# Kernel tuning notes

Hardware: AMD Instinct MI355X
Metric: run time of the kernel (lower is better)

The kernel has to match this reference:

```python
import jax, jax.numpy as jnp
import numpy as np

GAMMA = 1.0


def setup_inputs() -> dict:
    key = jax.random.key(0)
    kx, ky = jax.random.split(key)
    x = jax.random.normal(kx, (8192, 128), dtype=jnp.float32)
    y = jax.random.normal(ky, (8192, 128), dtype=jnp.float32)
    return {"x": x, "y": y}


def reference(x, y):
    # RBF kernel K[i,j] = exp(-gamma * ||x_i - y_j||^2)
    x2 = jnp.sum(x * x, axis=1)              # [N]
    y2 = jnp.sum(y * y, axis=1)              # [M]
    xy = jnp.einsum('nd,md->nm', x, y)       # [N, M] GEMM
    sq = x2[:, None] + y2[None, :] - 2.0 * xy
    sq = jnp.maximum(sq, 0.0)                # guard tiny negatives from cancellation
    return jnp.exp(-GAMMA * sq)
```

## Files before the change

### kernel.cpp

```cpp
#include <hip/hip_runtime.h>
#include <hip/hip_bf16.h>

typedef __bf16 bf16x8 __attribute__((ext_vector_type(8)));
typedef float f32x4 __attribute__((ext_vector_type(4)));
typedef unsigned short us4 __attribute__((ext_vector_type(4)));

#define NLOG2E -1.44269504088896340736f

__device__ __forceinline__ unsigned short f2bf(float f) {
    unsigned u = __float_as_uint(f);
    u += 0x7fffu + ((u >> 16) & 1u);
    return (unsigned short)(u >> 16);
}

__global__ __launch_bounds__(256)
void rbf_prep(const float* __restrict__ X, const float* __restrict__ Y,
              unsigned short* __restrict__ Xb, unsigned short* __restrict__ Yb,
              float* __restrict__ x2n, float* __restrict__ y2n) {
    const int b = blockIdx.x;
    const float* src = (b < 128) ? X : Y;
    unsigned short* db = (b < 128) ? Xb : Yb;
    float* dn = (b < 128) ? x2n : y2n;
    const int r0 = (b & 127) * 64;
    const int t = threadIdx.x;
    const f32x4* s4 = (const f32x4*)(src + (size_t)r0 * 128);
#pragma unroll
    for (int i = 0; i < 8; ++i) {
        int idx = i * 256 + t;
        int r = idx >> 5, c4 = idx & 31;
        f32x4 v = s4[idx];
        us4 o;
        o.x = f2bf(v[0]); o.y = f2bf(v[1]); o.z = f2bf(v[2]); o.w = f2bf(v[3]);
        int pc = (c4 >> 1) ^ (r & 7);
        *(us4*)&db[(size_t)(r0 + r) * 128 + pc * 8 + (c4 & 1) * 4] = o;
    }
    if (t < 64) {
        const f32x4* row = (const f32x4*)(src + (size_t)(r0 + t) * 128);
        float s = 0.f;
#pragma unroll
        for (int c = 0; c < 32; ++c) {
            f32x4 v = row[c];
            s += v[0] * v[0] + v[1] * v[1] + v[2] * v[2] + v[3] * v[3];
        }
        dn[r0 + t] = NLOG2E * s;
    }
}

__global__ __launch_bounds__(256, 5)
void rbf_main(const unsigned short* __restrict__ Xb, const unsigned short* __restrict__ Yb,
              const float* __restrict__ x2n, const float* __restrict__ y2n,
              float* __restrict__ O) {
    __shared__ __align__(16) char smem[32768];
    unsigned short* Ab = (unsigned short*)smem;
    unsigned short* Bb = (unsigned short*)(smem + 16384);

    const int t = threadIdx.x, l = t & 63, w = t >> 6;
    const int col0 = blockIdx.x * 64, row0 = blockIdx.y * 64;

    const char* gA = (const char*)(Xb + (size_t)row0 * 128);
    const char* gB = (const char*)(Yb + (size_t)col0 * 128);
#pragma unroll
    for (int j = 0; j < 4; ++j) {
        int base = (w * 4 + j) * 1024;
        __builtin_amdgcn_global_load_lds(
            (const __attribute__((address_space(1))) void*)(gA + base + l * 16),
            (__attribute__((address_space(3))) void*)(smem + base), 16, 0, 0);
        __builtin_amdgcn_global_load_lds(
            (const __attribute__((address_space(1))) void*)(gB + base + l * 16),
            (__attribute__((address_space(3))) void*)(smem + 16384 + base), 16, 0, 0);
    }

    const int lr = l & 15, q = l >> 4;
    const int wr = (w >> 1) * 32, wc = (w & 1) * 32;

    f32x4 xn[2]; float yn[2];
#pragma unroll
    for (int m = 0; m < 2; ++m) xn[m] = *(const f32x4*)&x2n[row0 + wr + m * 16 + q * 4];
#pragma unroll
    for (int n = 0; n < 2; ++n) yn[n] = y2n[col0 + wc + n * 16 + lr];

    __syncthreads();

    f32x4 acc[2][2] = {};
#pragma unroll
    for (int k = 0; k < 4; ++k) {
        bf16x8 af[2], bv[2];
#pragma unroll
        for (int m = 0; m < 2; ++m) {
            int R = wr + m * 16 + lr;
            af[m] = *(const bf16x8*)((const char*)Ab + R * 256 + (((k << 2) + q) ^ (R & 7)) * 16);
        }
#pragma unroll
        for (int n = 0; n < 2; ++n) {
            int R = wc + n * 16 + lr;
            bv[n] = *(const bf16x8*)((const char*)Bb + R * 256 + (((k << 2) + q) ^ (R & 7)) * 16);
        }
#pragma unroll
        for (int m = 0; m < 2; ++m)
#pragma unroll
            for (int n = 0; n < 2; ++n)
                acc[m][n] = __builtin_amdgcn_mfma_f32_16x16x32_bf16(af[m], bv[n], acc[m][n], 0, 0, 0);
    }

    __syncthreads();

    float* Ol = (float*)(smem + w * 4096);
#pragma unroll
    for (int m = 0; m < 2; ++m) {
#pragma unroll
        for (int n = 0; n < 2; ++n) {
            int col = n * 16 + lr;
            int lc = col >> 2;
            float ynv = yn[n];
#pragma unroll
            for (int i = 0; i < 4; ++i) {
                int row = m * 16 + q * 4 + i;
                float arg = fmaf(-2.0f * NLOG2E, acc[m][n][i], xn[m][i] + ynv);
                arg = fminf(arg, 0.f);
                int pc = (lc ^ row) & 7;
                Ol[row * 32 + pc * 4 + (col & 3)] = exp2f(arg);
            }
        }
    }

#pragma unroll
    for (int it = 0; it < 4; ++it) {
        int r = it * 8 + (l >> 3);
        int lc2 = l & 7;
        int pc = lc2 ^ (r & 7);
        f32x4 v = *(const f32x4*)((const char*)Ol + r * 128 + pc * 16);
        *(float4*)&O[(size_t)(row0 + wr + r) * 8192 + col0 + wc + lc2 * 4] = *(float4*)&v;
    }
}

extern "C" void kernel_launch(void* const* d_in, const int* in_sizes, int n_in,
                              void* d_out, int out_size, void* d_ws, size_t ws_size,
                              hipStream_t stream) {
    const float* X = (const float*)d_in[0];
    const float* Y = (const float*)d_in[1];
    float* O = (float*)d_out;
    const int N = in_sizes[0] / 128;
    const int M = in_sizes[1] / 128;
    unsigned short* Xb = (unsigned short*)d_ws;
    unsigned short* Yb = Xb + (size_t)N * 128;
    float* x2n = (float*)(Yb + (size_t)M * 128);
    float* y2n = x2n + N;
    rbf_prep<<<dim3((N + M) / 64), 256, 0, stream>>>(X, Y, Xb, Yb, x2n, y2n);
    rbf_main<<<dim3(M / 64, N / 64), 256, 0, stream>>>(Xb, Yb, x2n, y2n, O);
}
```

Before: 285.2 us.

## Widen output tile to 64x128 with 32x32 MFMA and direct stores

Each block now covers 128 columns instead of 64, and the GEMM switches from 16x16x32 MFMAs to 32x32x16 MFMAs so one A fragment is reused across two B fragments. The LDS-staged transposed output write is removed. Results are stored straight from the MFMA accumulator layout as 32 consecutive floats per row segment. This cuts LDS traffic, one barrier and the per-block setup, at the cost of more shared memory, lower occupancy (launch bound 3) and possibly less coalesced stores.

```diff
diff --git a/kernel.cpp b/kernel.cpp
--- a/kernel.cpp
+++ b/kernel.cpp
@@ -3,9 +3,11 @@
 
 typedef __bf16 bf16x8 __attribute__((ext_vector_type(8)));
 typedef float f32x4 __attribute__((ext_vector_type(4)));
+typedef float f32x16 __attribute__((ext_vector_type(16)));
 typedef unsigned short us4 __attribute__((ext_vector_type(4)));
 
-#define NLOG2E -1.44269504088896340736f
+#define NLOG2E  -1.44269504088896340736f
+#define TWOLOG2E 2.88539008177792681472f
 
 __device__ __forceinline__ unsigned short f2bf(float f) {
     unsigned u = __float_as_uint(f);
@@ -46,16 +48,14 @@
     }
 }
 
-__global__ __launch_bounds__(256, 5)
+__global__ __launch_bounds__(256, 3)
 void rbf_main(const unsigned short* __restrict__ Xb, const unsigned short* __restrict__ Yb,
               const float* __restrict__ x2n, const float* __restrict__ y2n,
-              float* __restrict__ O) {
-    __shared__ __align__(16) char smem[32768];
-    unsigned short* Ab = (unsigned short*)smem;
-    unsigned short* Bb = (unsigned short*)(smem + 16384);
+              float* __restrict__ O, int ldo) {
+    __shared__ __align__(16) char smem[49152];
 
     const int t = threadIdx.x, l = t & 63, w = t >> 6;
-    const int col0 = blockIdx.x * 64, row0 = blockIdx.y * 64;
+    const int col0 = blockIdx.x * 128, row0 = blockIdx.y * 64;
 
     const char* gA = (const char*)(Xb + (size_t)row0 * 128);
     const char* gB = (const char*)(Yb + (size_t)col0 * 128);
@@ -65,71 +65,57 @@
         __builtin_amdgcn_global_load_lds(
             (const __attribute__((address_space(1))) void*)(gA + base + l * 16),
             (__attribute__((address_space(3))) void*)(smem + base), 16, 0, 0);
+    }
+#pragma unroll
+    for (int j = 0; j < 8; ++j) {
+        int base = (w * 8 + j) * 1024;
         __builtin_amdgcn_global_load_lds(
             (const __attribute__((address_space(1))) void*)(gB + base + l * 16),
             (__attribute__((address_space(3))) void*)(smem + 16384 + base), 16, 0, 0);
     }
 
-    const int lr = l & 15, q = l >> 4;
-    const int wr = (w >> 1) * 32, wc = (w & 1) * 32;
+    const int ln = l & 31, hi = l >> 5;
+    const int wr = (w >> 1) * 32, wcw = (w & 1) * 64;
 
-    f32x4 xn[2]; float yn[2];
+    f32x4 xv[4];
 #pragma unroll
-    for (int m = 0; m < 2; ++m) xn[m] = *(const f32x4*)&x2n[row0 + wr + m * 16 + q * 4];
+    for (int g = 0; g < 4; ++g)
+        xv[g] = *(const f32x4*)&x2n[row0 + wr + 8 * g + 4 * hi];
+    float ynp[2];
 #pragma unroll
-    for (int n = 0; n < 2; ++n) yn[n] = y2n[col0 + wc + n * 16 + lr];
+    for (int nf = 0; nf < 2; ++nf)
+        ynp[nf] = y2n[col0 + wcw + nf * 32 + ln];
 
     __syncthreads();
 
-    f32x4 acc[2][2] = {};
+    f32x16 acc0 = {}, acc1 = {};
+    const int RA = wr + ln;
+    const int C0 = wcw + ln;
+    const int C1 = wcw + 32 + ln;
 #pragma unroll
-    for (int k = 0; k < 4; ++k) {
-        bf16x8 af[2], bv[2];
-#pragma unroll
-        for (int m = 0; m < 2; ++m) {
-            int R = wr + m * 16 + lr;
-            af[m] = *(const bf16x8*)((const char*)Ab + R * 256 + (((k << 2) + q) ^ (R & 7)) * 16);
-        }
-#pragma unroll
-        for (int n = 0; n < 2; ++n) {
-            int R = wc + n * 16 + lr;
-            bv[n] = *(const bf16x8*)((const char*)Bb + R * 256 + (((k << 2) + q) ^ (R & 7)) * 16);
-        }
-#pragma unroll
-        for (int m = 0; m < 2; ++m)
-#pragma unroll
-            for (int n = 0; n < 2; ++n)
-                acc[m][n] = __builtin_amdgcn_mfma_f32_16x16x32_bf16(af[m], bv[n], acc[m][n], 0, 0, 0);
-    }
-
-    __syncthreads();
-
-    float* Ol = (float*)(smem + w * 4096);
-#pragma unroll
-    for (int m = 0; m < 2; ++m) {
-#pragma unroll
-        for (int n = 0; n < 2; ++n) {
-            int col = n * 16 + lr;
-            int lc = col >> 2;
-            float ynv = yn[n];
-#pragma unroll
-            for (int i = 0; i < 4; ++i) {
-                int row = m * 16 + q * 4 + i;
-                float arg = fmaf(-2.0f * NLOG2E, acc[m][n][i], xn[m][i] + ynv);
-                arg = fminf(arg, 0.f);
-                int pc = (lc ^ row) & 7;
-                Ol[row * 32 + pc * 4 + (col & 3)] = exp2f(arg);
-            }
-        }
+    for (int kk = 0; kk < 8; ++kk) {
+        int lc = 2 * kk + hi;
+        bf16x8 af = *(const bf16x8*)(smem + RA * 256 + ((lc ^ (RA & 7)) * 16));
+        bf16x8 b0 = *(const bf16x8*)(smem + 16384 + C0 * 256 + ((lc ^ (C0 & 7)) * 16));
+        bf16x8 b1 = *(const bf16x8*)(smem + 16384 + C1 * 256 + ((lc ^ (C1 & 7)) * 16));
+        acc0 = __builtin_amdgcn_mfma_f32_32x32x16_bf16(af, b0, acc0, 0, 0, 0);
+        acc1 = __builtin_amdgcn_mfma_f32_32x32x16_bf16(af, b1, acc1, 0, 0, 0);
     }
 
 #pragma unroll
-    for (int it = 0; it < 4; ++it) {
-        int r = it * 8 + (l >> 3);
-        int lc2 = l & 7;
-        int pc = lc2 ^ (r & 7);
-        f32x4 v = *(const f32x4*)((const char*)Ol + r * 128 + pc * 16);
-        *(float4*)&O[(size_t)(row0 + wr + r) * 8192 + col0 + wc + lc2 * 4] = *(float4*)&v;
+    for (int nf = 0; nf < 2; ++nf) {
+        float yb = ynp[nf];
+        float* ob = &O[(size_t)(row0 + wr + 4 * hi) * ldo + col0 + wcw + nf * 32 + ln];
+#pragma unroll
+        for (int g = 0; g < 4; ++g) {
+#pragma unroll
+            for (int i = 0; i < 4; ++i) {
+                float xy = (nf == 0) ? acc0[g * 4 + i] : acc1[g * 4 + i];
+                float arg = fmaf(TWOLOG2E, xy, xv[g][i] + yb);
+                arg = fminf(arg, 0.f);
+                ob[(size_t)(8 * g + i) * ldo] = exp2f(arg);
+            }
+        }
     }
 }
 
@@ -146,5 +132,5 @@
     float* x2n = (float*)(Yb + (size_t)M * 128);
     float* y2n = x2n + N;
     rbf_prep<<<dim3((N + M) / 64), 256, 0, stream>>>(X, Y, Xb, Yb, x2n, y2n);
-    rbf_main<<<dim3(M / 64, N / 64), 256, 0, stream>>>(Xb, Yb, x2n, y2n, O);
+    rbf_main<<<dim3(M / 128, N / 64), 256, 0, stream>>>(Xb, Yb, x2n, y2n, O, M);
 }
```

New measurement: 269.9 us. 1.06x faster.
